# Kernel optimization log

Hardware: AMD Instinct MI355X
Metric: run time of the kernel (lower is better)

Reference implementation:

```python
import jax, jax.numpy as jnp
import numpy as np
import math

D_MODEL = 768
N_HEADS = 12
D_HEAD = D_MODEL // N_HEADS
B, T = 2, 2048
EPS = 1e-5


def _layernorm(x, g, b):
    mu = jnp.mean(x, axis=-1, keepdims=True)
    var = jnp.var(x, axis=-1, keepdims=True)
    return (x - mu) * jax.lax.rsqrt(var + EPS) * g + b


def setup_inputs() -> dict:
    key = jax.random.key(0)
    ks = jax.random.split(key, 16)
    s = 0.02
    inp = {
        "x": jax.random.normal(ks[0], (B, T, D_MODEL), jnp.float32),
        "q_pos": jax.random.normal(ks[1], (B, N_HEADS, T, D_HEAD), jnp.float32),
        "k_pos": jax.random.normal(ks[2], (B, N_HEADS, T, D_HEAD), jnp.float32),
        "causal_mask": jnp.triu(jnp.ones((T, T), dtype=bool), k=1),
        "Wq": jax.random.normal(ks[3], (D_MODEL, D_MODEL), jnp.float32) * s,
        "bq": jnp.zeros((D_MODEL,), jnp.float32),
        "Wk": jax.random.normal(ks[4], (D_MODEL, D_MODEL), jnp.float32) * s,
        "bk": jnp.zeros((D_MODEL,), jnp.float32),
        "Wv": jax.random.normal(ks[5], (D_MODEL, D_MODEL), jnp.float32) * s,
        "bv": jnp.zeros((D_MODEL,), jnp.float32),
        "Wo": jax.random.normal(ks[6], (D_MODEL, D_MODEL), jnp.float32) * s,
        "bo": jnp.zeros((D_MODEL,), jnp.float32),
        "ln1_g": jnp.ones((D_MODEL,), jnp.float32),
        "ln1_b": jnp.zeros((D_MODEL,), jnp.float32),
        "ln2_g": jnp.ones((D_MODEL,), jnp.float32),
        "ln2_b": jnp.zeros((D_MODEL,), jnp.float32),
        "W1": jax.random.normal(ks[7], (D_MODEL, 4 * D_MODEL), jnp.float32) * s,
        "b1": jnp.zeros((4 * D_MODEL,), jnp.float32),
        "W2": jax.random.normal(ks[8], (4 * D_MODEL, D_MODEL), jnp.float32) * s,
        "b2": jnp.zeros((D_MODEL,), jnp.float32),
    }
    return inp


def reference(x, q_pos, k_pos, causal_mask, Wq, bq, Wk, bk, Wv, bv, Wo, bo,
              ln1_g, ln1_b, ln2_g, ln2_b, W1, b1, W2, b2):
    h = _layernorm(x, ln1_g, ln1_b)  # [B,T,D]
    # project and split heads -> [B,H,T,d]
    def heads(y):
        return y.reshape(B, T, N_HEADS, D_HEAD).transpose(0, 2, 1, 3)
    Qc = heads(h @ Wq + bq)
    Kc = heads(h @ Wk + bk)
    V = heads(h @ Wv + bv)
    scale = math.sqrt(D_HEAD)
    A_X = jnp.einsum('bhqd,bhkd->bhqk', Qc, Kc) / scale
    A_P = jnp.einsum('bhqd,bhkd->bhqk', q_pos, k_pos) / scale
    scores = A_X * A_P  # Hadamard combination of content + positional scores
    scores = jnp.where(causal_mask[None, None, :, :], -jnp.inf, scores)
    attn = jax.nn.softmax(scores, axis=-1)
    out = jnp.einsum('bhqk,bhkd->bhqd', attn, V)  # [B,H,T,d]
    out = out.transpose(0, 2, 1, 3).reshape(B, T, D_MODEL)
    out = out @ Wo + bo
    x = x + out
    h2 = _layernorm(x, ln2_g, ln2_b)
    ffn = jax.nn.gelu(h2 @ W1 + b1, approximate=False) @ W2 + b2
    return x + ffn
```

## Files before the change

kernel.cpp:

```cpp
#include <hip/hip_runtime.h>
#include <hip/hip_bf16.h>
#include <math.h>

#define D_MODEL 768
#define N_HEADS 12
#define D_HEAD  64
#define BATCH   2
#define SEQ     2048
#define ROWS    (BATCH*SEQ)
#define D_FFN   (4*D_MODEL)

typedef short bf16x8 __attribute__((ext_vector_type(8)));
typedef float f32x4  __attribute__((ext_vector_type(4)));

__device__ __forceinline__ short f2bf(float f) {
    __hip_bfloat16 h = __float2bfloat16(f);
    return *reinterpret_cast<short*>(&h);
}

template<int CTRL>
__device__ __forceinline__ float dpp_f(float x) {
    int v = __builtin_amdgcn_update_dpp(0, __float_as_int(x), CTRL, 0xF, 0xF, true);
    return __int_as_float(v);
}
__device__ __forceinline__ float dpp_max16(float x) {
    x = fmaxf(x, dpp_f<0xB1>(x));
    x = fmaxf(x, dpp_f<0x4E>(x));
    x = fmaxf(x, dpp_f<0x141>(x));
    x = fmaxf(x, dpp_f<0x140>(x));
    return x;
}
__device__ __forceinline__ float dpp_sum16(float x) {
    x += dpp_f<0xB1>(x);
    x += dpp_f<0x4E>(x);
    x += dpp_f<0x141>(x);
    x += dpp_f<0x140>(x);
    return x;
}

__global__ __launch_bounds__(256)
void prep_kernel(const float* __restrict__ Wq, const float* __restrict__ Wk,
                 const float* __restrict__ Wv, const float* __restrict__ Wo,
                 const float* __restrict__ W1, const float* __restrict__ W2,
                 const float* __restrict__ q_pos, const float* __restrict__ k_pos,
                 const float* __restrict__ x, const float* __restrict__ ln1_g,
                 const float* __restrict__ ln1_b,
                 short* __restrict__ WTq, short* __restrict__ WTk,
                 short* __restrict__ WTv, short* __restrict__ WTo,
                 short* __restrict__ WT1, short* __restrict__ WT2,
                 short* __restrict__ qp_bf, short* __restrict__ kp_bf,
                 short* __restrict__ h_bf) {
    int id = blockIdx.x;
    if (id >= 9984) {
        int row = id - 9984;
        const float* xr = x + (size_t)row * D_MODEL;
        int t = threadIdx.x;
        float v0 = xr[t], v1 = xr[t + 256], v2 = xr[t + 512];
        float s  = v0 + v1 + v2;
        float s2 = v0*v0 + v1*v1 + v2*v2;
        __shared__ float rs[4], rs2[4];
        #pragma unroll
        for (int off = 32; off; off >>= 1) {
            s  += __shfl_down(s, off);
            s2 += __shfl_down(s2, off);
        }
        int wv = t >> 6, ln = t & 63;
        if (ln == 0) { rs[wv] = s; rs2[wv] = s2; }
        __syncthreads();
        float S  = rs[0] + rs[1] + rs[2] + rs[3];
        float S2 = rs2[0] + rs2[1] + rs2[2] + rs2[3];
        float mu  = S * (1.0f / D_MODEL);
        float var = S2 * (1.0f / D_MODEL) - mu * mu;
        float inv = rsqrtf(var + 1e-5f);
        short* orow = h_bf + (size_t)row * D_MODEL;
        orow[t]       = f2bf((v0 - mu) * inv * ln1_g[t]       + ln1_b[t]);
        orow[t + 256] = f2bf((v1 - mu) * inv * ln1_g[t + 256] + ln1_b[t + 256]);
        orow[t + 512] = f2bf((v2 - mu) * inv * ln1_g[t + 512] + ln1_b[t + 512]);
        return;
    }
    if (id >= 6912) {
        int cid = id - 6912;
        bool isq = (cid < 1536);
        int c = isq ? cid : cid - 1536;
        const float* src = isq ? q_pos : k_pos;
        short* dst = isq ? qp_bf : kp_bf;
        float sc = isq ? 0.125f : 1.0f;
        int i = (c * 256 + threadIdx.x) * 8;
        float4 a = *reinterpret_cast<const float4*>(src + i);
        float4 b = *reinterpret_cast<const float4*>(src + i + 4);
        bf16x8 r;
        r[0]=f2bf(a.x*sc); r[1]=f2bf(a.y*sc); r[2]=f2bf(a.z*sc); r[3]=f2bf(a.w*sc);
        r[4]=f2bf(b.x*sc); r[5]=f2bf(b.y*sc); r[6]=f2bf(b.z*sc); r[7]=f2bf(b.w*sc);
        *reinterpret_cast<bf16x8*>(dst + i) = r;
        return;
    }
    const float* W; short* WT; int K, N, t;
    if (id < 576)        { W = Wq; WT = WTq; K = 768;  N = 768;  t = id; }
    else if (id < 1152)  { W = Wk; WT = WTk; K = 768;  N = 768;  t = id - 576; }
    else if (id < 1728)  { W = Wv; WT = WTv; K = 768;  N = 768;  t = id - 1152; }
    else if (id < 2304)  { W = Wo; WT = WTo; K = 768;  N = 768;  t = id - 1728; }
    else if (id < 4608)  { W = W1; WT = WT1; K = 768;  N = 3072; t = id - 2304; }
    else                 { W = W2; WT = WT2; K = 3072; N = 768;  t = id - 4608; }
    int nb = N >> 5;
    int n0 = (t % nb) * 32, k0 = (t / nb) * 32;
    __shared__ float tile[32][33];
    int tx = threadIdx.x & 31, ty = threadIdx.x >> 5;
    #pragma unroll
    for (int i = 0; i < 4; ++i)
        tile[ty + 8*i][tx] = W[(size_t)(k0 + ty + 8*i) * N + n0 + tx];
    __syncthreads();
    #pragma unroll
    for (int i = 0; i < 4; ++i)
        WT[(size_t)(n0 + ty + 8*i) * K + k0 + tx] = f2bf(tile[tx][ty + 8*i]);
}

__global__ __launch_bounds__(256)
void transpose_v_kernel(const short* __restrict__ Vm, short* __restrict__ Vt) {
    __shared__ short tile[64][72];
    int kt = blockIdx.x;
    int bh = blockIdx.y;
    int b = bh / N_HEADS, h = bh % N_HEADS;
    int tid = threadIdx.x;
    int row = tid >> 2, c16 = (tid & 3) * 16;
    const short* src = Vm + ((size_t)(b * SEQ) + kt * 64 + row) * D_MODEL + h * 64 + c16;
    *reinterpret_cast<bf16x8*>(&tile[row][c16])     = *reinterpret_cast<const bf16x8*>(src);
    *reinterpret_cast<bf16x8*>(&tile[row][c16 + 8]) = *reinterpret_cast<const bf16x8*>(src + 8);
    __syncthreads();
    int d = tid >> 2, k16 = (tid & 3) * 16;
    short o[16];
    #pragma unroll
    for (int j = 0; j < 16; ++j) o[j] = tile[k16 + j][d];
    short* dst = Vt + ((size_t)bh * 64 + d) * SEQ + kt * 64 + k16;
    *reinterpret_cast<bf16x8*>(dst)     = *reinterpret_cast<bf16x8*>(&o[0]);
    *reinterpret_cast<bf16x8*>(dst + 8) = *reinterpret_cast<bf16x8*>(&o[8]);
}

__global__ __launch_bounds__(256)
void ln2_fuse_kernel(const float* __restrict__ P0, const float* __restrict__ P1,
                     const float* __restrict__ bo, const float* __restrict__ x,
                     const float* __restrict__ g, const float* __restrict__ beta,
                     float* __restrict__ x2, short* __restrict__ out) {
    int row = blockIdx.x;
    size_t base = (size_t)row * D_MODEL;
    int t = threadIdx.x;
    float v0 = P0[base + t]       + P1[base + t]       + bo[t]       + x[base + t];
    float v1 = P0[base + t + 256] + P1[base + t + 256] + bo[t + 256] + x[base + t + 256];
    float v2 = P0[base + t + 512] + P1[base + t + 512] + bo[t + 512] + x[base + t + 512];
    x2[base + t] = v0; x2[base + t + 256] = v1; x2[base + t + 512] = v2;
    float s  = v0 + v1 + v2;
    float s2 = v0*v0 + v1*v1 + v2*v2;
    __shared__ float rs[4], rs2[4];
    #pragma unroll
    for (int off = 32; off; off >>= 1) {
        s  += __shfl_down(s, off);
        s2 += __shfl_down(s2, off);
    }
    int wv = t >> 6, ln = t & 63;
    if (ln == 0) { rs[wv] = s; rs2[wv] = s2; }
    __syncthreads();
    float S  = rs[0] + rs[1] + rs[2] + rs[3];
    float S2 = rs2[0] + rs2[1] + rs2[2] + rs2[3];
    float mu  = S * (1.0f / D_MODEL);
    float var = S2 * (1.0f / D_MODEL) - mu * mu;
    float inv = rsqrtf(var + 1e-5f);
    short* orow = out + base;
    orow[t]       = f2bf((v0 - mu) * inv * g[t]       + beta[t]);
    orow[t + 256] = f2bf((v1 - mu) * inv * g[t + 256] + beta[t + 256]);
    orow[t + 512] = f2bf((v2 - mu) * inv * g[t + 512] + beta[t + 512]);
}

template<int ACT, bool RES, bool OUTBF>
__device__ __forceinline__
void gemm_body(const short* __restrict__ A, const short* __restrict__ WT,
               const float* __restrict__ bias, const float* __restrict__ res,
               void* __restrict__ Cout, int M, int N, int Kloop, int Kstride,
               float oscale) {
    __shared__ short As[2][128 * 32];
    __shared__ short Bs[2][128 * 32];
    const int tid = threadIdx.x;
    const int w = tid >> 6, lane = tid & 63;
    const int lr = lane & 15, lg = lane >> 4;
    const int wm = w >> 1, wn = w & 1;
    const int bm = blockIdx.y * 128, bn = blockIdx.x * 128;

    f32x4 acc[4][4] = {};

    const int srow = w * 32 + (lane >> 2);
    const int scol = (lane & 3) * 8;
    const short* Ag = A  + (size_t)(bm + srow) * Kstride + scol;
    const short* Bg = WT + (size_t)(bn + srow) * Kstride + scol;

    auto stage = [&](int k0, int buf) {
        #pragma unroll
        for (int r = 0; r < 2; ++r) {
            __builtin_amdgcn_global_load_lds(
                (const __attribute__((address_space(1))) void*)(Ag + (size_t)r * 16 * Kstride + k0),
                (__attribute__((address_space(3))) void*)(&As[buf][0] + w * 1024 + r * 512),
                16, 0, 0);
            __builtin_amdgcn_global_load_lds(
                (const __attribute__((address_space(1))) void*)(Bg + (size_t)r * 16 * Kstride + k0),
                (__attribute__((address_space(3))) void*)(&Bs[buf][0] + w * 1024 + r * 512),
                16, 0, 0);
        }
    };

    stage(0, 0);
    __syncthreads();
    int cur = 0;

    for (int k0 = 0; k0 < Kloop; k0 += 32) {
        if (k0 + 32 < Kloop) stage(k0 + 32, cur ^ 1);

        bf16x8 af[4], bfr[4];
        #pragma unroll
        for (int mi = 0; mi < 4; ++mi)
            af[mi] = *reinterpret_cast<const bf16x8*>(&As[cur][0] + (wm*64 + mi*16 + lr) * 32 + lg*8);
        #pragma unroll
        for (int nj = 0; nj < 4; ++nj)
            bfr[nj] = *reinterpret_cast<const bf16x8*>(&Bs[cur][0] + (wn*64 + nj*16 + lr) * 32 + lg*8);
        __builtin_amdgcn_s_setprio(1);
        #pragma unroll
        for (int mi = 0; mi < 4; ++mi)
            #pragma unroll
            for (int nj = 0; nj < 4; ++nj)
                acc[mi][nj] = __builtin_amdgcn_mfma_f32_16x16x32_bf16(af[mi], bfr[nj], acc[mi][nj], 0, 0, 0);
        __builtin_amdgcn_s_setprio(0);

        __syncthreads();
        cur ^= 1;
    }

    float bias_v[4] = {0.f, 0.f, 0.f, 0.f};
    if constexpr (ACT != 2) {
        #pragma unroll
        for (int nj = 0; nj < 4; ++nj) bias_v[nj] = bias[bn + wn*64 + nj*16 + lr];
    }

    #pragma unroll
    for (int mi = 0; mi < 4; ++mi) {
        #pragma unroll
        for (int j = 0; j < 4; ++j) {
            size_t m = bm + wm*64 + mi*16 + lg*4 + j;
            #pragma unroll
            for (int nj = 0; nj < 4; ++nj) {
                size_t n = bn + wn*64 + nj*16 + lr;
                float v = acc[mi][nj][j] + bias_v[nj];
                if (RES) v += res[m * N + n];
                if (ACT == 1) v = 0.5f * v * (1.0f + erff(v * 0.70710678118f));
                if (OUTBF) ((short*)Cout)[m * N + n] = f2bf(v * oscale);
                else       ((float*)Cout)[m * N + n] = v;
            }
        }
    }
}

template<int ACT, bool RES, bool OUTBF>
__global__ __launch_bounds__(256)
void gemm_mfma_kernel(const short* __restrict__ A, const short* __restrict__ WT,
                      const float* __restrict__ bias, const float* __restrict__ res,
                      void* __restrict__ Cout, int M, int N, int K) {
    gemm_body<ACT, RES, OUTBF>(A, WT, bias, res, Cout, M, N, K, K, 1.0f);
}

__global__ __launch_bounds__(256)
void gemm_qkv_kernel(const short* __restrict__ A,
                     const short* __restrict__ WTq, const short* __restrict__ WTk,
                     const short* __restrict__ WTv,
                     const float* __restrict__ bq, const float* __restrict__ bk,
                     const float* __restrict__ bv,
                     short* __restrict__ Qm, short* __restrict__ Km, short* __restrict__ Vm) {
    const short* WT; const float* bias; short* C; float sc;
    if (blockIdx.z == 0)      { WT = WTq; bias = bq; C = Qm; sc = 0.125f; }
    else if (blockIdx.z == 1) { WT = WTk; bias = bk; C = Km; sc = 1.0f; }
    else                      { WT = WTv; bias = bv; C = Vm; sc = 1.0f; }
    gemm_body<0, false, true>(A, WT, bias, nullptr, C, ROWS, D_MODEL, D_MODEL, D_MODEL, sc);
}

__global__ __launch_bounds__(256)
void gemm_wo_kernel(const short* __restrict__ ao, const short* __restrict__ WTo,
                    float* __restrict__ P0, float* __restrict__ P1) {
    int z = blockIdx.z;
    gemm_body<2, false, false>(ao + z * 384, WTo + z * 384, nullptr, nullptr,
                               z ? P1 : P0, ROWS, D_MODEL, 384, D_MODEL, 1.0f);
}

__global__ __launch_bounds__(256)
void gemm_w2_kernel(const short* __restrict__ mid, const short* __restrict__ WT2,
                    float* __restrict__ P0, float* __restrict__ P1) {
    int z = blockIdx.z;
    gemm_body<2, false, false>(mid + z * 1536, WT2 + z * 1536, nullptr, nullptr,
                               z ? P1 : P0, ROWS, D_MODEL, 1536, D_FFN, 1.0f);
}

__global__ __launch_bounds__(256)
void w2_epi_kernel(const float* __restrict__ P0, const float* __restrict__ P1,
                   const float* __restrict__ b2, const float* __restrict__ x2,
                   float* __restrict__ out) {
    size_t i = ((size_t)blockIdx.x * 256 + threadIdx.x) * 4;
    int n = (int)(i % D_MODEL);
    float4 p0 = *reinterpret_cast<const float4*>(P0 + i);
    float4 p1 = *reinterpret_cast<const float4*>(P1 + i);
    float4 xr = *reinterpret_cast<const float4*>(x2 + i);
    float4 bb = *reinterpret_cast<const float4*>(b2 + n);
    float4 o;
    o.x = p0.x + p1.x + xr.x + bb.x;
    o.y = p0.y + p1.y + xr.y + bb.y;
    o.z = p0.z + p1.z + xr.z + bb.z;
    o.w = p0.w + p1.w + xr.w + bb.w;
    *reinterpret_cast<float4*>(out + i) = o;
}

__global__ __launch_bounds__(128)
void attn_mfma_kernel(const short* __restrict__ Q, const short* __restrict__ K,
                      const short* __restrict__ Vt, const short* __restrict__ qp,
                      const short* __restrict__ kp, short* __restrict__ ao) {
    __shared__ short Ks[2][4096];
    __shared__ short kps[2][4096];
    __shared__ short Vts[2][4096];
    __shared__ short Plds[2][16][72];

    int lin = blockIdx.x;
    int wid = (lin & 7) * 96 + (lin >> 3);
    int bh = wid >> 5;
    int pair = wid & 31;
    int b = bh / N_HEADS, h = bh % N_HEADS;
    int tid = threadIdx.x, w = tid >> 6, lane = tid & 63;
    int lr = lane & 15, lg = lane >> 4;

    const short* Kh  = K  + (size_t)(b * SEQ) * D_MODEL + h * 64;
    const short* kph = kp + (size_t)bh * SEQ * 64;
    const short* Vth = Vt + (size_t)bh * 64 * SEQ;

    const int s_sub  = lane >> 3;
    const int s_colb = ((lane & 7) ^ s_sub) << 4;

    auto stage = [&](int kt, int buf) {
        #pragma unroll
        for (int j = 0; j < 4; ++j) {
            int row = (w * 4 + j) * 8 + s_sub;
            int ldsoff = (w * 4 + j) * 1024;
            __builtin_amdgcn_global_load_lds(
                (const __attribute__((address_space(1))) void*)
                    ((const char*)(Kh + (size_t)(kt * 64 + row) * D_MODEL) + s_colb),
                (__attribute__((address_space(3))) void*)((char*)&Ks[buf][0] + ldsoff), 16, 0, 0);
            __builtin_amdgcn_global_load_lds(
                (const __attribute__((address_space(1))) void*)
                    ((const char*)(kph + (size_t)(kt * 64 + row) * 64) + s_colb),
                (__attribute__((address_space(3))) void*)((char*)&kps[buf][0] + ldsoff), 16, 0, 0);
            __builtin_amdgcn_global_load_lds(
                (const __attribute__((address_space(1))) void*)
                    ((const char*)(Vth + (size_t)row * SEQ + kt * 64) + s_colb),
                (__attribute__((address_space(3))) void*)((char*)&Vts[buf][0] + ldsoff), 16, 0, 0);
        }
    };
    auto ldr = [&](const short* base, int row, int halfb) -> bf16x8 {
        int off = row * 128 + ((halfb + lg * 16) ^ ((row & 7) << 4));
        return *reinterpret_cast<const bf16x8*>((const char*)base + off);
    };

    #pragma unroll
    for (int ph = 0; ph < 2; ++ph) {
        int qt = ph ? 63 - pair : pair;
        int qbase = qt * 32 + w * 16;

        const short* Qrow  = Q  + ((size_t)(b * SEQ) + qbase + lr) * D_MODEL + h * 64;
        const short* qprow = qp + ((size_t)bh * SEQ + qbase + lr) * 64;
        bf16x8 qf0  = *reinterpret_cast<const bf16x8*>(Qrow + lg * 8);
        bf16x8 qf1  = *reinterpret_cast<const bf16x8*>(Qrow + 32 + lg * 8);
        bf16x8 qpf0 = *reinterpret_cast<const bf16x8*>(qprow + lg * 8);
        bf16x8 qpf1 = *reinterpret_cast<const bf16x8*>(qprow + 32 + lg * 8);

        f32x4 o_acc[4] = {};
        float m_run[4], l_run[4];
        #pragma unroll
        for (int r = 0; r < 4; ++r) { m_run[r] = -1e30f; l_run[r] = 0.f; }

        int nkt = qt / 2 + 1;
        stage(0, 0);
        __syncthreads();
        int cur = 0;

        for (int kt = 0; kt < nkt; ++kt) {
            if (kt + 1 < nkt) stage(kt + 1, cur ^ 1);

            const short* Kb  = &Ks[cur][0];
            const short* kpb = &kps[cur][0];
            const short* Vb  = &Vts[cur][0];
            f32x4 sx[4] = {}, sp[4] = {};
            __builtin_amdgcn_s_setprio(1);
            #pragma unroll
            for (int sub = 0; sub < 4; ++sub) {
                int row = sub * 16 + lr;
                bf16x8 kf0 = ldr(Kb, row, 0),  kf1 = ldr(Kb, row, 64);
                bf16x8 kq0 = ldr(kpb, row, 0), kq1 = ldr(kpb, row, 64);
                sx[sub] = __builtin_amdgcn_mfma_f32_16x16x32_bf16(qf0,  kf0, sx[sub], 0, 0, 0);
                sx[sub] = __builtin_amdgcn_mfma_f32_16x16x32_bf16(qf1,  kf1, sx[sub], 0, 0, 0);
                sp[sub] = __builtin_amdgcn_mfma_f32_16x16x32_bf16(qpf0, kq0, sp[sub], 0, 0, 0);
                sp[sub] = __builtin_amdgcn_mfma_f32_16x16x32_bf16(qpf1, kq1, sp[sub], 0, 0, 0);
            }
            __builtin_amdgcn_s_setprio(0);

            float sc[4][4];
            float pmax[4];
            bool diag = (kt == nkt - 1);
            #pragma unroll
            for (int r = 0; r < 4; ++r) {
                int row = qbase + lg * 4 + r;
                float mx = -1e30f;
                #pragma unroll
                for (int sub = 0; sub < 4; ++sub) {
                    float v = sx[sub][r] * sp[sub][r];
                    if (diag) {
                        int col = kt * 64 + sub * 16 + lr;
                        if (col > row) v = -1e30f;
                    }
                    sc[sub][r] = v;
                    mx = fmaxf(mx, v);
                }
                pmax[r] = dpp_max16(mx);
            }

            bool need = false;
            #pragma unroll
            for (int r = 0; r < 4; ++r) need = need || (pmax[r] > m_run[r] + 8.f);
            if (__any(need)) {
                #pragma unroll
                for (int r = 0; r < 4; ++r) {
                    float m_new = fmaxf(m_run[r], pmax[r]);
                    float scale = __expf(m_run[r] - m_new);
                    m_run[r] = m_new;
                    l_run[r] *= scale;
                    #pragma unroll
                    for (int ds = 0; ds < 4; ++ds) o_acc[ds][r] *= scale;
                }
            }
            #pragma unroll
            for (int r = 0; r < 4; ++r) {
                float s = 0.f;
                #pragma unroll
                for (int sub = 0; sub < 4; ++sub) {
                    float pv = __expf(sc[sub][r] - m_run[r]);
                    sc[sub][r] = pv;
                    s += pv;
                }
                l_run[r] += dpp_sum16(s);
            }

            #pragma unroll
            for (int sub = 0; sub < 4; ++sub)
                #pragma unroll
                for (int r = 0; r < 4; ++r)
                    Plds[w][lg * 4 + r][sub * 16 + lr] = f2bf(sc[sub][r]);

            bf16x8 pa0 = *reinterpret_cast<bf16x8*>(&Plds[w][lr][lg * 8]);
            bf16x8 pa1 = *reinterpret_cast<bf16x8*>(&Plds[w][lr][32 + lg * 8]);

            __builtin_amdgcn_s_setprio(1);
            #pragma unroll
            for (int ds = 0; ds < 4; ++ds) {
                int row = ds * 16 + lr;
                bf16x8 vb0 = ldr(Vb, row, 0), vb1 = ldr(Vb, row, 64);
                o_acc[ds] = __builtin_amdgcn_mfma_f32_16x16x32_bf16(pa0, vb0, o_acc[ds], 0, 0, 0);
                o_acc[ds] = __builtin_amdgcn_mfma_f32_16x16x32_bf16(pa1, vb1, o_acc[ds], 0, 0, 0);
            }
            __builtin_amdgcn_s_setprio(0);

            __syncthreads();
            cur ^= 1;
        }

        #pragma unroll
        for (int ds = 0; ds < 4; ++ds)
            #pragma unroll
            for (int r = 0; r < 4; ++r) {
                int row = qbase + lg * 4 + r;
                float val = o_acc[ds][r] / l_run[r];
                ao[((size_t)(b * SEQ) + row) * D_MODEL + h * 64 + ds * 16 + lr] = f2bf(val);
            }
        __syncthreads();
    }
}

extern "C" void kernel_launch(void* const* d_in, const int* in_sizes, int n_in,
                              void* d_out, int out_size, void* d_ws, size_t ws_size,
                              hipStream_t stream) {
    const float* x     = (const float*)d_in[0];
    const float* q_pos = (const float*)d_in[1];
    const float* k_pos = (const float*)d_in[2];
    const float* Wq = (const float*)d_in[4];
    const float* bq = (const float*)d_in[5];
    const float* Wk = (const float*)d_in[6];
    const float* bk = (const float*)d_in[7];
    const float* Wv = (const float*)d_in[8];
    const float* bv = (const float*)d_in[9];
    const float* Wo = (const float*)d_in[10];
    const float* bo = (const float*)d_in[11];
    const float* ln1_g = (const float*)d_in[12];
    const float* ln1_b = (const float*)d_in[13];
    const float* ln2_g = (const float*)d_in[14];
    const float* ln2_b = (const float*)d_in[15];
    const float* W1 = (const float*)d_in[16];
    const float* b1 = (const float*)d_in[17];
    const float* W2 = (const float*)d_in[18];
    const float* b2 = (const float*)d_in[19];
    float* out = (float*)d_out;

    char* p = (char*)d_ws;
    auto alloc = [&](size_t bytes) { char* q = p; p += (bytes + 255) & ~(size_t)255; return q; };
    const size_t SA = (size_t)ROWS * D_MODEL;
    const size_t SP = (size_t)BATCH * N_HEADS * SEQ * 64;

    short* h_bf  = (short*)alloc(SA * 2);
    short* Qm    = (short*)alloc(SA * 2);
    short* Km    = (short*)alloc(SA * 2);
    short* Vm    = (short*)alloc(SA * 2);
    short* Vt    = (short*)alloc(SP * 2);
    short* ao    = (short*)alloc(SA * 2);
    short* qp_bf = (short*)alloc(SP * 2);
    short* kp_bf = (short*)alloc(SP * 2);
    short* mid   = (short*)alloc((size_t)ROWS * D_FFN * 2);
    float* x2    = (float*)alloc(SA * 4);
    float* P0    = (float*)alloc(SA * 4);
    float* P1    = (float*)alloc(SA * 4);
    short* WTq   = (short*)alloc((size_t)D_MODEL * D_MODEL * 2);
    short* WTk   = (short*)alloc((size_t)D_MODEL * D_MODEL * 2);
    short* WTv   = (short*)alloc((size_t)D_MODEL * D_MODEL * 2);
    short* WTo   = (short*)alloc((size_t)D_MODEL * D_MODEL * 2);
    short* WT1   = (short*)alloc((size_t)D_MODEL * D_FFN * 2);
    short* WT2   = (short*)alloc((size_t)D_MODEL * D_FFN * 2);

    prep_kernel<<<14080, 256, 0, stream>>>(Wq, Wk, Wv, Wo, W1, W2, q_pos, k_pos,
                                           x, ln1_g, ln1_b,
                                           WTq, WTk, WTv, WTo, WT1, WT2,
                                           qp_bf, kp_bf, h_bf);

    gemm_qkv_kernel<<<dim3(D_MODEL/128, ROWS/128, 3), 256, 0, stream>>>(
        h_bf, WTq, WTk, WTv, bq, bk, bv, Qm, Km, Vm);
    transpose_v_kernel<<<dim3(SEQ/64, BATCH*N_HEADS), 256, 0, stream>>>(Vm, Vt);
    attn_mfma_kernel<<<768, 128, 0, stream>>>(Qm, Km, Vt, qp_bf, kp_bf, ao);
    gemm_wo_kernel<<<dim3(D_MODEL/128, ROWS/128, 2), 256, 0, stream>>>(ao, WTo, P0, P1);
    ln2_fuse_kernel<<<ROWS, 256, 0, stream>>>(P0, P1, bo, x, ln2_g, ln2_b, x2, h_bf);
    gemm_mfma_kernel<1, false, true><<<dim3(D_FFN/128, ROWS/128), 256, 0, stream>>>(
        h_bf, WT1, b1, nullptr, mid, ROWS, D_FFN, D_MODEL);
    gemm_w2_kernel<<<dim3(D_MODEL/128, ROWS/128, 2), 256, 0, stream>>>(mid, WT2, P0, P1);
    w2_epi_kernel<<<(int)(SA/1024), 256, 0, stream>>>(P0, P1, b2, x2, out);
}
```

Measured before the change: 223.2 us.

## Load positional keys directly to registers and fold log2e into Q scaling

Removes the shared-memory double buffer for the positional keys (kp) in the attention kernel. Each warp now reads its kp fragments straight from global memory into registers at the top of every key tile, which shrinks the LDS footprint and is paired with a launch-bounds occupancy hint. The Q and q_pos pre-scale becomes sqrt(log2 e)/8, so the score product carries a log2 e factor and the softmax uses exp2f instead of __expf. The cost is that the kp global loads are not prefetched and may stall on latency. The online-softmax rescale threshold now effectively operates in the base-2 domain.

```diff
diff --git a/kernel.cpp b/kernel.cpp
--- a/kernel.cpp
+++ b/kernel.cpp
@@ -37,6 +37,8 @@
     x += dpp_f<0x140>(x);
     return x;
 }
+
+#define QSCALE 0.15014031f
 
 __global__ __launch_bounds__(256)
 void prep_kernel(const float* __restrict__ Wq, const float* __restrict__ Wk,
@@ -84,7 +86,7 @@
         int c = isq ? cid : cid - 1536;
         const float* src = isq ? q_pos : k_pos;
         short* dst = isq ? qp_bf : kp_bf;
-        float sc = isq ? 0.125f : 1.0f;
+        float sc = isq ? QSCALE : 1.0f;
         int i = (c * 256 + threadIdx.x) * 8;
         float4 a = *reinterpret_cast<const float4*>(src + i);
         float4 b = *reinterpret_cast<const float4*>(src + i + 4);
@@ -270,7 +272,7 @@
                      const float* __restrict__ bv,
                      short* __restrict__ Qm, short* __restrict__ Km, short* __restrict__ Vm) {
     const short* WT; const float* bias; short* C; float sc;
-    if (blockIdx.z == 0)      { WT = WTq; bias = bq; C = Qm; sc = 0.125f; }
+    if (blockIdx.z == 0)      { WT = WTq; bias = bq; C = Qm; sc = QSCALE; }
     else if (blockIdx.z == 1) { WT = WTk; bias = bk; C = Km; sc = 1.0f; }
     else                      { WT = WTv; bias = bv; C = Vm; sc = 1.0f; }
     gemm_body<0, false, true>(A, WT, bias, nullptr, C, ROWS, D_MODEL, D_MODEL, D_MODEL, sc);
@@ -310,12 +312,11 @@
     *reinterpret_cast<float4*>(out + i) = o;
 }
 
-__global__ __launch_bounds__(128)
+__global__ __launch_bounds__(128, 2)
 void attn_mfma_kernel(const short* __restrict__ Q, const short* __restrict__ K,
                       const short* __restrict__ Vt, const short* __restrict__ qp,
                       const short* __restrict__ kp, short* __restrict__ ao) {
     __shared__ short Ks[2][4096];
-    __shared__ short kps[2][4096];
     __shared__ short Vts[2][4096];
     __shared__ short Plds[2][16][72];
 
@@ -343,10 +344,6 @@
                 (const __attribute__((address_space(1))) void*)
                     ((const char*)(Kh + (size_t)(kt * 64 + row) * D_MODEL) + s_colb),
                 (__attribute__((address_space(3))) void*)((char*)&Ks[buf][0] + ldsoff), 16, 0, 0);
-            __builtin_amdgcn_global_load_lds(
-                (const __attribute__((address_space(1))) void*)
-                    ((const char*)(kph + (size_t)(kt * 64 + row) * 64) + s_colb),
-                (__attribute__((address_space(3))) void*)((char*)&kps[buf][0] + ldsoff), 16, 0, 0);
             __builtin_amdgcn_global_load_lds(
                 (const __attribute__((address_space(1))) void*)
                     ((const char*)(Vth + (size_t)row * SEQ + kt * 64) + s_colb),
@@ -381,22 +378,30 @@
         int cur = 0;
 
         for (int kt = 0; kt < nkt; ++kt) {
+            bf16x8 kq[4][2];
+            #pragma unroll
+            for (int sub = 0; sub < 4; ++sub) {
+                const short* kpr = kph + (size_t)(kt * 64 + sub * 16 + lr) * 64;
+                kq[sub][0] = *reinterpret_cast<const bf16x8*>(kpr + lg * 8);
+                kq[sub][1] = *reinterpret_cast<const bf16x8*>(kpr + 32 + lg * 8);
+            }
             if (kt + 1 < nkt) stage(kt + 1, cur ^ 1);
 
-            const short* Kb  = &Ks[cur][0];
-            const short* kpb = &kps[cur][0];
-            const short* Vb  = &Vts[cur][0];
+            const short* Kb = &Ks[cur][0];
+            const short* Vb = &Vts[cur][0];
             f32x4 sx[4] = {}, sp[4] = {};
             __builtin_amdgcn_s_setprio(1);
             #pragma unroll
             for (int sub = 0; sub < 4; ++sub) {
                 int row = sub * 16 + lr;
-                bf16x8 kf0 = ldr(Kb, row, 0),  kf1 = ldr(Kb, row, 64);
-                bf16x8 kq0 = ldr(kpb, row, 0), kq1 = ldr(kpb, row, 64);
-                sx[sub] = __builtin_amdgcn_mfma_f32_16x16x32_bf16(qf0,  kf0, sx[sub], 0, 0, 0);
-                sx[sub] = __builtin_amdgcn_mfma_f32_16x16x32_bf16(qf1,  kf1, sx[sub], 0, 0, 0);
-                sp[sub] = __builtin_amdgcn_mfma_f32_16x16x32_bf16(qpf0, kq0, sp[sub], 0, 0, 0);
-                sp[sub] = __builtin_amdgcn_mfma_f32_16x16x32_bf16(qpf1, kq1, sp[sub], 0, 0, 0);
+                bf16x8 kf0 = ldr(Kb, row, 0), kf1 = ldr(Kb, row, 64);
+                sx[sub] = __builtin_amdgcn_mfma_f32_16x16x32_bf16(qf0, kf0, sx[sub], 0, 0, 0);
+                sx[sub] = __builtin_amdgcn_mfma_f32_16x16x32_bf16(qf1, kf1, sx[sub], 0, 0, 0);
+            }
+            #pragma unroll
+            for (int sub = 0; sub < 4; ++sub) {
+                sp[sub] = __builtin_amdgcn_mfma_f32_16x16x32_bf16(qpf0, kq[sub][0], sp[sub], 0, 0, 0);
+                sp[sub] = __builtin_amdgcn_mfma_f32_16x16x32_bf16(qpf1, kq[sub][1], sp[sub], 0, 0, 0);
             }
             __builtin_amdgcn_s_setprio(0);
 
@@ -427,7 +432,7 @@
                 #pragma unroll
                 for (int r = 0; r < 4; ++r) {
                     float m_new = fmaxf(m_run[r], pmax[r]);
-                    float scale = __expf(m_run[r] - m_new);
+                    float scale = exp2f(m_run[r] - m_new);
                     m_run[r] = m_new;
                     l_run[r] *= scale;
                     #pragma unroll
@@ -439,7 +444,7 @@
                 float s = 0.f;
                 #pragma unroll
                 for (int sub = 0; sub < 4; ++sub) {
-                    float pv = __expf(sc[sub][r] - m_run[r]);
+                    float pv = exp2f(sc[sub][r] - m_run[r]);
                     sc[sub][r] = pv;
                     s += pv;
                 }
```

Result: slower. 240.8 us (+7.9%).
